# Kernel tuning notes

Measured on AMD Instinct MI355X. Metric: run time of the kernel, lower is better.

Reference implementation:

```python
import jax, jax.numpy as jnp
import numpy as np

WS = (4, 4, 4)      # window size (d, h, w)
SS = (2, 2, 2)      # shift size
HEADS = 4
EPS = 1e-6          # flax LayerNorm default epsilon


def _rel_pos_index(ws):
    # replicates the source exactly (np.meshgrid default 'xy' indexing)
    coords = np.stack(np.meshgrid(np.arange(ws[0]), np.arange(ws[1]), np.arange(ws[2])))
    cf = coords.reshape(3, -1)
    rc = (cf[:, :, None] - cf[:, None, :]).transpose(1, 2, 0).astype(np.int64)
    rc[:, :, 0] += ws[0] - 1
    rc[:, :, 1] += ws[1] - 1
    rc[:, :, 2] += ws[2] - 1
    rc[:, :, 0] *= (2 * ws[1] - 1) * (2 * ws[2] - 1)
    rc[:, :, 1] *= 2 * ws[2] - 1
    return rc.sum(-1)  # (n, n)


def _compute_mask(dp, hp, wp, ws, ss):
    # standard shifted-window attention mask: (nw, n, n) with 0 / -100
    img = np.zeros((1, dp, hp, wp, 1), np.float32)
    cnt = 0
    sls = lambda w, s: (slice(0, -w), slice(-w, -s), slice(-s, None))
    for d in sls(ws[0], ss[0]):
        for h in sls(ws[1], ss[1]):
            for w in sls(ws[2], ss[2]):
                img[:, d, h, w, :] = cnt
                cnt += 1
    mw = img.reshape(1, dp // ws[0], ws[0], hp // ws[1], ws[1], wp // ws[2], ws[2], 1)
    mw = mw.transpose(0, 1, 3, 5, 2, 4, 6, 7).reshape(-1, ws[0] * ws[1] * ws[2])
    am = mw[:, None, :] - mw[:, :, None]
    return np.where(am != 0, np.float32(-100.0), np.float32(0.0))


def window_partition(x, ws):
    b, d, h, w, c = x.shape
    x = x.reshape(b, d // ws[0], ws[0], h // ws[1], ws[1], w // ws[2], ws[2], c)
    return x.transpose(0, 1, 3, 5, 2, 4, 6, 7).reshape(-1, ws[0] * ws[1] * ws[2], c)


def window_reverse(windows, ws, dims):
    b, d, h, w = dims
    x = windows.reshape(b, d // ws[0], h // ws[1], w // ws[2], ws[0], ws[1], ws[2], -1)
    return x.transpose(0, 1, 4, 2, 5, 3, 6, 7).reshape(b, d, h, w, -1)


def layernorm(x, scale, bias):
    m = x.mean(-1, keepdims=True)
    v = x.var(-1, keepdims=True)
    return (x - m) * jax.lax.rsqrt(v + EPS) * scale + bias


def setup_inputs() -> dict:
    key = jax.random.key(0)
    ks = jax.random.split(key, 8)
    B, D, H, W, C = 2, 32, 64, 64, 128
    HID = 4 * C
    p = 0.02
    return {
        "x": jax.random.normal(ks[0], (B, D, H, W, C), jnp.float32),
        "mask": jnp.asarray(_compute_mask(D, H, W, WS, SS)),
        "norm1_scale": jnp.ones((C,), jnp.float32),
        "norm1_bias": jnp.zeros((C,), jnp.float32),
        "qkv_w": jax.random.normal(ks[1], (C, 3 * C), jnp.float32) * p,
        "rel_bias_table": jax.random.normal(ks[2], ((2 * WS[0] - 1) * (2 * WS[1] - 1) * (2 * WS[2] - 1), HEADS), jnp.float32) * p,
        "proj_w": jax.random.normal(ks[3], (C, C), jnp.float32) * p,
        "proj_b": jnp.zeros((C,), jnp.float32),
        "norm2_scale": jnp.ones((C,), jnp.float32),
        "norm2_bias": jnp.zeros((C,), jnp.float32),
        "mlp_w1": jax.random.normal(ks[4], (C, HID), jnp.float32) * p,
        "mlp_b1": jnp.zeros((HID,), jnp.float32),
        "mlp_w2": jax.random.normal(ks[5], (HID, C), jnp.float32) * p,
        "mlp_b2": jnp.zeros((C,), jnp.float32),
    }


def reference(x, mask, norm1_scale, norm1_bias, qkv_w, rel_bias_table, proj_w, proj_b,
              norm2_scale, norm2_bias, mlp_w1, mlp_b1, mlp_w2, mlp_b2):
    b, d, h, w, c = x.shape
    hd = c // HEADS
    scale = hd ** -0.5
    n = WS[0] * WS[1] * WS[2]

    shortcut = x
    xn = layernorm(x, norm1_scale, norm1_bias)
    # cyclic shift + window partition
    shifted = jnp.roll(xn, shift=(-SS[0], -SS[1], -SS[2]), axis=(1, 2, 3))
    xw = window_partition(shifted, WS)                      # (b*nw, n, c)
    bw = xw.shape[0]

    qkv = (xw @ qkv_w).reshape(bw, n, 3, HEADS, hd).transpose(2, 0, 3, 1, 4)
    q, k, v = qkv[0] * scale, qkv[1], qkv[2]                # (bw, heads, n, hd)
    attn = jnp.einsum('bhqd,bhkd->bhqk', q, k)              # (bw, heads, n, n)

    idx = _rel_pos_index(WS)
    bias = rel_bias_table[idx.reshape(-1)].reshape(n, n, HEADS).transpose(2, 0, 1)
    attn = attn + bias[None]

    nw = mask.shape[0]
    attn = attn.reshape(bw // nw, nw, HEADS, n, n) + mask[None, :, None]
    attn = jax.nn.softmax(attn.reshape(bw, HEADS, n, n), axis=-1)

    out = jnp.einsum('bhqk,bhkd->bhqd', attn, v)
    out = jnp.swapaxes(out, 1, 2).reshape(bw, n, c)
    out = out @ proj_w + proj_b

    attn_out = window_reverse(out, WS, (b, d, h, w))
    attn_out = jnp.roll(attn_out, shift=SS, axis=(1, 2, 3))

    x = shortcut + attn_out
    xn2 = layernorm(x, norm2_scale, norm2_bias)
    m = jax.nn.gelu(xn2 @ mlp_w1 + mlp_b1) @ mlp_w2 + mlp_b2
    return x + m
```

## Files before the change

kernel.cpp:

```cpp
#include <hip/hip_runtime.h>

typedef __bf16 bf16x8 __attribute__((ext_vector_type(8)));
typedef float f32x4 __attribute__((ext_vector_type(4)));
typedef unsigned short u16x4 __attribute__((ext_vector_type(4)));
typedef unsigned short u16x8 __attribute__((ext_vector_type(8)));

#define MFMA16(a,b,c) __builtin_amdgcn_mfma_f32_16x16x32_bf16((a),(b),(c),0,0,0)

__device__ __forceinline__ unsigned short f2bf(float f){
  return __builtin_bit_cast(unsigned short, static_cast<__bf16>(f));
}
__device__ __forceinline__ float bf2f(unsigned short h){
  unsigned u = ((unsigned)h)<<16;
  return __builtin_bit_cast(float, u);
}
__device__ __forceinline__ bf16x8 g_frag(const unsigned short* __restrict__ wf, int fragIdx, int lane){
  return __builtin_bit_cast(bf16x8, *reinterpret_cast<const u16x8*>(wf + (size_t)(fragIdx*64 + lane)*8));
}
__device__ __forceinline__ bf16x8 lds_frag(const unsigned short* base, int fragIdx, int lane){
  return __builtin_bit_cast(bf16x8, *reinterpret_cast<const u16x8*>(base + (fragIdx*64 + lane)*8));
}
__device__ __forceinline__ bf16x8 bc(u16x8 v){ return __builtin_bit_cast(bf16x8, v); }

__device__ __forceinline__ void pack_body(const float* __restrict__ src, unsigned short* __restrict__ dst,
                                          int blk, int MT, int KP, int M){
  int tid = blk*256 + threadIdx.x;
  if (tid >= MT*KP*64) return;
  int lane = tid & 63;
  int t2 = tid >> 6;
  int kp = t2 % KP;
  int m = 16*(t2 / KP) + (lane & 15);
  int g = lane >> 4;
  u16x8 v;
#pragma unroll
  for (int j = 0; j < 8; ++j) {
    int k = 4*g + (j&3) + 16*(j>>2) + 32*kp;
    v[j] = f2bf(src[k*M + m]);
  }
  *reinterpret_cast<u16x8*>(&dst[(size_t)tid*8]) = v;
}

__global__ void prep_kernel(const float* __restrict__ qkvw, const float* __restrict__ pw,
                            const float* __restrict__ w1, const float* __restrict__ w2,
                            const float* __restrict__ tbl,
                            unsigned short* __restrict__ wqk_f, unsigned short* __restrict__ wvb_f,
                            unsigned short* __restrict__ wproj_f,
                            unsigned short* __restrict__ w1_f, unsigned short* __restrict__ w2_f,
                            float* __restrict__ bias2){
  const int bb = blockIdx.x;
  if (bb < 16)      { pack_body(qkvw,       wqk_f,   bb,      16, 4, 384); return; }
  else if (bb < 24) { pack_body(qkvw + 256, wvb_f,   bb-16,    8, 4, 384); return; }
  else if (bb < 32) { pack_body(pw,         wproj_f, bb-24,    8, 4, 128); return; }
  else if (bb < 64) { pack_body(w1,         w1_f,    bb-32,   32, 4, 512); return; }
  else if (bb < 96) { pack_body(w2,         w2_f,    bb-64,    8,16, 128); return; }
  const int o = (bb-96)*256 + threadIdx.x;
  int r2 = o&3, lane = (o>>2)&63, nt = (o>>8)&3, mt = (o>>10)&3, h = o>>12;
  int g = lane>>4, l15 = lane&15;
  int key = 16*mt + 4*g + r2, q = 16*nt + l15;
  int da = ((q>>2)&3) - ((key>>2)&3) + 3;
  int ha = (q>>4)     - (key>>4)     + 3;
  int wa = (q&3)      - (key&3)      + 3;
  bias2[o] = tbl[((da*7+ha)*7+wa)*4 + h];
}

__global__ __launch_bounds__(256, 3)
void swin_block_kernel(const float* __restrict__ x,
                       const float* __restrict__ n1s, const float* __restrict__ n1b,
                       const unsigned short* __restrict__ wqk,
                       const unsigned short* __restrict__ wvb,
                       const float* __restrict__ bias2,
                       const unsigned short* __restrict__ wproj,
                       const float* __restrict__ projb,
                       const float* __restrict__ n2s, const float* __restrict__ n2b,
                       const unsigned short* __restrict__ w1f, const float* __restrict__ b1,
                       const unsigned short* __restrict__ w2f, const float* __restrict__ b2,
                       float* __restrict__ out)
{
  __shared__ __align__(16) unsigned short ldsA[16*64*8];
  __shared__ __align__(16) unsigned short ldsH[16*64*8];
  __shared__ int rid_s[64];

  const int tid  = threadIdx.x;
  const int lane = tid & 63;
  const int w    = tid >> 6;
  const int g    = lane >> 4;
  const int l15  = lane & 15;

  const int wb = blockIdx.x;
  const int b  = wb >> 11;
  const int r0 = wb & 2047;
  const int bd = r0 >> 8, bh = (r0 >> 4) & 15, bwi = r0 & 15;
  const bool edge = (bd==7) || (bh==15) || (bwi==15);

  const int t = tid >> 2, qtr = tid & 3;
  const int wd = t >> 4, wh = (t >> 2) & 3, ww = t & 3;
  const int dco = (bd*4 + wd + 2) & 31;
  const int hco = (bh*4 + wh + 2) & 63;
  const int wco = (bwi*4 + ww + 2) & 63;
  const long tokl = ((long)((b*32 + dco)*64 + hco))*64 + wco;
  const float* xrow = x + tokl*128 + qtr*32;
  const int tileT = t >> 4, l15t = t & 15;

  u16x8 rsd[4];
  {
    float xr[32];
    float s = 0.f, sq = 0.f;
#pragma unroll
    for (int i = 0; i < 8; ++i) {
      float4 v = reinterpret_cast<const float4*>(xrow)[i];
      xr[4*i+0]=v.x; xr[4*i+1]=v.y; xr[4*i+2]=v.z; xr[4*i+3]=v.w;
      s  += v.x + v.y + v.z + v.w;
      sq += v.x*v.x + v.y*v.y + v.z*v.z + v.w*v.w;
    }
    s  += __shfl_xor(s, 1);  s  += __shfl_xor(s, 2);
    sq += __shfl_xor(sq, 1); sq += __shfl_xor(sq, 2);
    const float mean = s * 0.0078125f;
    const float rs   = rsqrtf(sq * 0.0078125f - mean*mean + 1e-6f);
#pragma unroll
    for (int i = 0; i < 8; ++i) {
      u16x4 o4;
#pragma unroll
      for (int j2 = 0; j2 < 4; ++j2) {
        int c = qtr*32 + 4*i + j2;
        o4[j2] = f2bf((xr[4*i+j2]-mean)*rs*n1s[c] + n1b[c]);
        rsd[i>>1][4*(i&1)+j2] = f2bf(xr[4*i+j2]);
      }
      *reinterpret_cast<u16x4*>(&ldsA[((tileT*4+qtr)*64 + l15t + 16*(i&3))*8 + 4*(i>>2)]) = o4;
    }
  }
  if (edge && tid < 64) {
    int twd = tid >> 4, twh = (tid >> 2) & 3, tww = tid & 3;
    int rd = (bd == 7)  ? (twd < 2 ? 1 : 2) : 0;
    int rh = (bh == 15) ? (twh < 2 ? 1 : 2) : 0;
    int rw = (bwi == 15)? (tww < 2 ? 1 : 2) : 0;
    rid_s[tid] = rd*9 + rh*3 + rw;
  }
  __syncthreads();

  u16x8 Qf[4], Kf[4], Vf[2][2];
  {
    f32x4 qacc[2][4], kacc[2][4], vacc[4][2];
#pragma unroll
    for (int a2=0;a2<2;++a2)
#pragma unroll
      for (int b4=0;b4<4;++b4){ f32x4 z={0.f,0.f,0.f,0.f}; qacc[a2][b4]=z; kacc[a2][b4]=z; vacc[b4][a2]=z; }
#pragma unroll
    for (int kp=0;kp<4;++kp){
      bf16x8 fx[4];
#pragma unroll
      for (int nt=0;nt<4;++nt) fx[nt] = lds_frag(ldsA, nt*4+kp, lane);
#pragma unroll
      for (int mi=0;mi<2;++mi){
        bf16x8 aq = g_frag(wqk, (2*w+mi)*4+kp, lane);
#pragma unroll
        for (int nt=0;nt<4;++nt) qacc[mi][nt] = MFMA16(aq, fx[nt], qacc[mi][nt]);
      }
#pragma unroll
      for (int mi=0;mi<2;++mi){
        bf16x8 ak = g_frag(wqk, (8+2*w+mi)*4+kp, lane);
#pragma unroll
        for (int nt=0;nt<4;++nt) kacc[mi][nt] = MFMA16(ak, fx[nt], kacc[mi][nt]);
      }
#pragma unroll
      for (int c2=0;c2<2;++c2){
        bf16x8 bv = g_frag(wvb, (2*w+c2)*4+kp, lane);
#pragma unroll
        for (int mt=0;mt<4;++mt) vacc[mt][c2] = MFMA16(fx[mt], bv, vacc[mt][c2]);
      }
    }
#pragma unroll
    for (int nt=0;nt<4;++nt){
      u16x8 vq, vk;
#pragma unroll
      for (int j=0;j<8;++j){
        vq[j] = f2bf(qacc[j>>2][nt][j&3]*0.17677669529663687f);
        vk[j] = f2bf(kacc[j>>2][nt][j&3]);
      }
      Qf[nt]=vq; Kf[nt]=vk;
    }
#pragma unroll
    for (int c2=0;c2<2;++c2)
#pragma unroll
      for (int kpk=0;kpk<2;++kpk){
        u16x8 v;
#pragma unroll
        for (int j=0;j<8;++j) v[j] = f2bf(vacc[(j>>2)+2*kpk][c2][j&3]);
        Vf[c2][kpk]=v;
      }
  }
  __syncthreads();

  {
    int4 rk[4];
    if (edge){
#pragma unroll
      for (int mt=0;mt<4;++mt) rk[mt] = *reinterpret_cast<const int4*>(&rid_s[16*mt + 4*g]);
    }
#pragma unroll
    for (int nt=0;nt<4;++nt){
      f32x4 sacc[4];
#pragma unroll
      for (int mt=0;mt<4;++mt){
        f32x4 z = {0.f,0.f,0.f,0.f};
        sacc[mt] = MFMA16(bc(Kf[mt]), bc(Qf[nt]), z);
      }
      if (edge){
        const int ridq = rid_s[16*nt + l15];
#pragma unroll
        for (int mt=0;mt<4;++mt){
          float4 bv = reinterpret_cast<const float4*>(bias2)[((w*4+mt)*4+nt)*64 + lane];
          sacc[mt][0] += bv.x + (rk[mt].x != ridq ? -100.f : 0.f);
          sacc[mt][1] += bv.y + (rk[mt].y != ridq ? -100.f : 0.f);
          sacc[mt][2] += bv.z + (rk[mt].z != ridq ? -100.f : 0.f);
          sacc[mt][3] += bv.w + (rk[mt].w != ridq ? -100.f : 0.f);
        }
      } else {
#pragma unroll
        for (int mt=0;mt<4;++mt){
          float4 bv = reinterpret_cast<const float4*>(bias2)[((w*4+mt)*4+nt)*64 + lane];
          sacc[mt][0] += bv.x; sacc[mt][1] += bv.y; sacc[mt][2] += bv.z; sacc[mt][3] += bv.w;
        }
      }
      float mx = -1e30f;
#pragma unroll
      for (int mt=0;mt<4;++mt)
#pragma unroll
        for (int r2=0;r2<4;++r2) mx = fmaxf(mx, sacc[mt][r2]);
      mx = fmaxf(mx, __shfl_xor(mx, 16));
      mx = fmaxf(mx, __shfl_xor(mx, 32));
      float sum = 0.f;
#pragma unroll
      for (int mt=0;mt<4;++mt)
#pragma unroll
        for (int r2=0;r2<4;++r2){
          float p = __expf(sacc[mt][r2] - mx);
          sacc[mt][r2] = p; sum += p;
        }
      sum += __shfl_xor(sum, 16);
      sum += __shfl_xor(sum, 32);
      const float inv = 1.f / sum;
      u16x8 Pf0, Pf1;
#pragma unroll
      for (int j=0;j<8;++j){
        Pf0[j] = f2bf(sacc[(j>>2)  ][j&3]*inv);
        Pf1[j] = f2bf(sacc[(j>>2)+2][j&3]*inv);
      }
      f32x4 oa[2];
#pragma unroll
      for (int c2=0;c2<2;++c2){
        f32x4 z = {0.f,0.f,0.f,0.f};
        z = MFMA16(bc(Vf[c2][0]), bc(Pf0), z);
        oa[c2] = MFMA16(bc(Vf[c2][1]), bc(Pf1), z);
      }
      u16x8 v;
#pragma unroll
      for (int j=0;j<8;++j) v[j] = f2bf(oa[j>>2][j&3]);
      *reinterpret_cast<u16x8*>(&ldsA[((nt*4+w)*64+lane)*8]) = v;
    }
  }
  __syncthreads();

  {
    f32x4 pacc[2][4];
#pragma unroll
    for (int mi=0;mi<2;++mi)
#pragma unroll
      for (int nt=0;nt<4;++nt){ f32x4 z={0.f,0.f,0.f,0.f}; pacc[mi][nt]=z; }
#pragma unroll
    for (int kp=0;kp<4;++kp){
      bf16x8 bo[4];
#pragma unroll
      for (int nt=0;nt<4;++nt) bo[nt] = lds_frag(ldsA, nt*4+kp, lane);
#pragma unroll
      for (int mi=0;mi<2;++mi){
        bf16x8 a = g_frag(wproj, (2*w+mi)*4+kp, lane);
#pragma unroll
        for (int nt=0;nt<4;++nt) pacc[mi][nt] = MFMA16(a, bo[nt], pacc[mi][nt]);
      }
    }
#pragma unroll
    for (int mi=0;mi<2;++mi)
#pragma unroll
      for (int r2=0;r2<4;++r2){
        const float pb = projb[16*(2*w+mi) + 4*g + r2];
#pragma unroll
        for (int nt=0;nt<4;++nt) pacc[mi][nt][r2] += pb;
      }
#pragma unroll
    for (int nt=0;nt<4;++nt){
      u16x8 v;
#pragma unroll
      for (int j=0;j<8;++j) v[j] = f2bf(pacc[j>>2][nt][j&3]);
      *reinterpret_cast<u16x8*>(&ldsH[((nt*4+w)*64+lane)*8]) = v;
    }
  }
  __syncthreads();

  {
    float xv[32];
    float s2 = 0.f, sq2 = 0.f;
#pragma unroll
    for (int i = 0; i < 8; ++i) {
      u16x4 sg = *reinterpret_cast<const u16x4*>(&ldsH[((tileT*4+qtr)*64 + l15t + 16*(i&3))*8 + 4*(i>>2)]);
#pragma unroll
      for (int j2 = 0; j2 < 4; ++j2) {
        float v2 = bf2f(rsd[i>>1][4*(i&1)+j2]) + bf2f(sg[j2]);
        xv[4*i+j2] = v2;
        s2 += v2; sq2 += v2*v2;
      }
    }
    s2  += __shfl_xor(s2, 1);  s2  += __shfl_xor(s2, 2);
    sq2 += __shfl_xor(sq2, 1); sq2 += __shfl_xor(sq2, 2);
    const float mean2 = s2*0.0078125f;
    const float rs2 = rsqrtf(sq2*0.0078125f - mean2*mean2 + 1e-6f);
#pragma unroll
    for (int i = 0; i < 8; ++i) {
      u16x4 o4;
#pragma unroll
      for (int j2 = 0; j2 < 4; ++j2) {
        int c = qtr*32 + 4*i + j2;
        o4[j2] = f2bf((xv[4*i+j2]-mean2)*rs2*n2s[c] + n2b[c]);
        rsd[i>>1][4*(i&1)+j2] = f2bf(xv[4*i+j2]);
      }
      *reinterpret_cast<u16x4*>(&ldsA[((tileT*4+qtr)*64 + l15t + 16*(i&3))*8 + 4*(i>>2)]) = o4;
    }
  }
  __syncthreads();

  {
    f32x4 macc[2][4];
#pragma unroll
    for (int mi=0;mi<2;++mi)
#pragma unroll
      for (int nt=0;nt<4;++nt){ f32x4 z={0.f,0.f,0.f,0.f}; macc[mi][nt]=z; }
#pragma unroll
    for (int cc=0;cc<4;++cc){
      f32x4 hacc[2][4];
#pragma unroll
      for (int mi=0;mi<2;++mi)
#pragma unroll
        for (int nt=0;nt<4;++nt){ f32x4 z={0.f,0.f,0.f,0.f}; hacc[mi][nt]=z; }
#pragma unroll
      for (int kp=0;kp<4;++kp){
        bf16x8 bn[4];
#pragma unroll
        for (int nt=0;nt<4;++nt) bn[nt] = lds_frag(ldsA, nt*4+kp, lane);
#pragma unroll
        for (int mi=0;mi<2;++mi){
          bf16x8 a = g_frag(w1f, (cc*8+2*w+mi)*4+kp, lane);
#pragma unroll
          for (int nt=0;nt<4;++nt) hacc[mi][nt] = MFMA16(a, bn[nt], hacc[mi][nt]);
        }
      }
#pragma unroll
      for (int nt=0;nt<4;++nt){
        u16x8 hv;
#pragma unroll
        for (int j=0;j<8;++j){
          const int mi = j>>2, r2 = j&3;
          const int hch = cc*128 + 32*w + 16*mi + 4*g + r2;
          float v2 = hacc[mi][nt][r2] + b1[hch];
          float gg = 0.7978845608028654f*(v2 + 0.044715f*v2*v2*v2);
          float ge = v2 / (1.f + __expf(-2.f*gg));
          hv[j] = f2bf(ge);
        }
        *reinterpret_cast<u16x8*>(&ldsH[((nt*4+w)*64+lane)*8]) = hv;
      }
      __syncthreads();
#pragma unroll
      for (int kph=0;kph<4;++kph){
        bf16x8 bhf[4];
#pragma unroll
        for (int nt=0;nt<4;++nt) bhf[nt] = lds_frag(ldsH, nt*4+kph, lane);
#pragma unroll
        for (int mi=0;mi<2;++mi){
          bf16x8 a2 = g_frag(w2f, (2*w+mi)*16 + cc*4 + kph, lane);
#pragma unroll
          for (int nt=0;nt<4;++nt) macc[mi][nt] = MFMA16(a2, bhf[nt], macc[mi][nt]);
        }
      }
      __syncthreads();
    }
#pragma unroll
    for (int nt=0;nt<4;++nt){
      u16x8 v;
#pragma unroll
      for (int j=0;j<8;++j){
        const int mi = j>>2, r2 = j&3;
        v[j] = f2bf(macc[mi][nt][r2] + b2[16*(2*w+mi) + 4*g + r2]);
      }
      *reinterpret_cast<u16x8*>(&ldsA[((nt*4+w)*64+lane)*8]) = v;
    }
  }
  __syncthreads();

  {
    float* orow = out + tokl*128 + qtr*32;
#pragma unroll
    for (int i = 0; i < 8; ++i) {
      u16x4 mv = *reinterpret_cast<const u16x4*>(&ldsA[((tileT*4+qtr)*64 + l15t + 16*(i&3))*8 + 4*(i>>2)]);
      float4 v;
      v.x = bf2f(rsd[i>>1][4*(i&1)+0]) + bf2f(mv[0]);
      v.y = bf2f(rsd[i>>1][4*(i&1)+1]) + bf2f(mv[1]);
      v.z = bf2f(rsd[i>>1][4*(i&1)+2]) + bf2f(mv[2]);
      v.w = bf2f(rsd[i>>1][4*(i&1)+3]) + bf2f(mv[3]);
      reinterpret_cast<float4*>(orow)[i] = v;
    }
  }
}

extern "C" void kernel_launch(void* const* d_in, const int* in_sizes, int n_in,
                              void* d_out, int out_size, void* d_ws, size_t ws_size,
                              hipStream_t stream) {
  (void)in_sizes; (void)n_in; (void)out_size; (void)ws_size;
  const float* x    = (const float*)d_in[0];
  const float* n1s  = (const float*)d_in[2];
  const float* n1b  = (const float*)d_in[3];
  const float* qkvw = (const float*)d_in[4];
  const float* tbl  = (const float*)d_in[5];
  const float* pw   = (const float*)d_in[6];
  const float* pb   = (const float*)d_in[7];
  const float* n2s  = (const float*)d_in[8];
  const float* n2b  = (const float*)d_in[9];
  const float* w1   = (const float*)d_in[10];
  const float* b1   = (const float*)d_in[11];
  const float* w2   = (const float*)d_in[12];
  const float* b2   = (const float*)d_in[13];
  float* out = (float*)d_out;

  unsigned short* wqk_f   = (unsigned short*)d_ws;
  unsigned short* wvb_f   = wqk_f   + 16*4*64*8;
  unsigned short* wproj_f = wvb_f   + 8*4*64*8;
  unsigned short* w1_f    = wproj_f + 8*4*64*8;
  unsigned short* w2_f    = w1_f    + 32*4*64*8;
  float*          bias2   = (float*)(w2_f + 8*16*64*8);

  prep_kernel<<<160, 256, 0, stream>>>(qkvw, pw, w1, w2, tbl,
                                       wqk_f, wvb_f, wproj_f, w1_f, w2_f, bias2);

  swin_block_kernel<<<4096, 256, 0, stream>>>(x, n1s, n1b, wqk_f, wvb_f, bias2, wproj_f, pb,
                                              n2s, n2b, w1_f, b1, w2_f, b2, out);
}
```

Before: 552.1 us.

## Split QKV projection into sequential phases and fold q-scale into weights

The fused Q/K/V projection loop, which held 24 accumulator tiles live at once, becomes three sequential phases that reuse one accumulator set, separated by scheduling barriers. The aim is to cut peak register pressure. The attention scale is folded into the packed Q weights during prep, so the kernel no longer multiplies per element. Launch bounds drop from 3 to 2 waves per EU, giving the compiler more registers at the cost of occupancy, and the LDS fragments are now reloaded three times instead of once.

```diff
diff --git a/kernel.cpp b/kernel.cpp
--- a/kernel.cpp
+++ b/kernel.cpp
@@ -23,7 +23,7 @@
 __device__ __forceinline__ bf16x8 bc(u16x8 v){ return __builtin_bit_cast(bf16x8, v); }
 
 __device__ __forceinline__ void pack_body(const float* __restrict__ src, unsigned short* __restrict__ dst,
-                                          int blk, int MT, int KP, int M){
+                                          int blk, int MT, int KP, int M, float scale){
   int tid = blk*256 + threadIdx.x;
   if (tid >= MT*KP*64) return;
   int lane = tid & 63;
@@ -35,7 +35,7 @@
 #pragma unroll
   for (int j = 0; j < 8; ++j) {
     int k = 4*g + (j&3) + 16*(j>>2) + 32*kp;
-    v[j] = f2bf(src[k*M + m]);
+    v[j] = f2bf(scale*src[k*M + m]);
   }
   *reinterpret_cast<u16x8*>(&dst[(size_t)tid*8]) = v;
 }
@@ -48,11 +48,12 @@
                             unsigned short* __restrict__ w1_f, unsigned short* __restrict__ w2_f,
                             float* __restrict__ bias2){
   const int bb = blockIdx.x;
-  if (bb < 16)      { pack_body(qkvw,       wqk_f,   bb,      16, 4, 384); return; }
-  else if (bb < 24) { pack_body(qkvw + 256, wvb_f,   bb-16,    8, 4, 384); return; }
-  else if (bb < 32) { pack_body(pw,         wproj_f, bb-24,    8, 4, 128); return; }
-  else if (bb < 64) { pack_body(w1,         w1_f,    bb-32,   32, 4, 512); return; }
-  else if (bb < 96) { pack_body(w2,         w2_f,    bb-64,    8,16, 128); return; }
+  if (bb < 8)       { pack_body(qkvw,       wqk_f,   bb,      16, 4, 384, 0.17677669529663687f); return; }
+  else if (bb < 16) { pack_body(qkvw,       wqk_f,   bb,      16, 4, 384, 1.f); return; }
+  else if (bb < 24) { pack_body(qkvw + 256, wvb_f,   bb-16,    8, 4, 384, 1.f); return; }
+  else if (bb < 32) { pack_body(pw,         wproj_f, bb-24,    8, 4, 128, 1.f); return; }
+  else if (bb < 64) { pack_body(w1,         w1_f,    bb-32,   32, 4, 512, 1.f); return; }
+  else if (bb < 96) { pack_body(w2,         w2_f,    bb-64,    8,16, 128, 1.f); return; }
   const int o = (bb-96)*256 + threadIdx.x;
   int r2 = o&3, lane = (o>>2)&63, nt = (o>>8)&3, mt = (o>>10)&3, h = o>>12;
   int g = lane>>4, l15 = lane&15;
@@ -63,7 +64,7 @@
   bias2[o] = tbl[((da*7+ha)*7+wa)*4 + h];
 }
 
-__global__ __launch_bounds__(256, 3)
+__global__ __launch_bounds__(256, 2)
 void swin_block_kernel(const float* __restrict__ x,
                        const float* __restrict__ n1s, const float* __restrict__ n1b,
                        const unsigned short* __restrict__ wqk,
@@ -139,11 +140,11 @@
 
   u16x8 Qf[4], Kf[4], Vf[2][2];
   {
-    f32x4 qacc[2][4], kacc[2][4], vacc[4][2];
-#pragma unroll
-    for (int a2=0;a2<2;++a2)
-#pragma unroll
-      for (int b4=0;b4<4;++b4){ f32x4 z={0.f,0.f,0.f,0.f}; qacc[a2][b4]=z; kacc[a2][b4]=z; vacc[b4][a2]=z; }
+    f32x4 acc[2][4];
+#pragma unroll
+    for (int mi=0;mi<2;++mi)
+#pragma unroll
+      for (int nt=0;nt<4;++nt){ f32x4 z={0.f,0.f,0.f,0.f}; acc[mi][nt]=z; }
 #pragma unroll
     for (int kp=0;kp<4;++kp){
       bf16x8 fx[4];
@@ -151,16 +152,53 @@
       for (int nt=0;nt<4;++nt) fx[nt] = lds_frag(ldsA, nt*4+kp, lane);
 #pragma unroll
       for (int mi=0;mi<2;++mi){
-        bf16x8 aq = g_frag(wqk, (2*w+mi)*4+kp, lane);
-#pragma unroll
-        for (int nt=0;nt<4;++nt) qacc[mi][nt] = MFMA16(aq, fx[nt], qacc[mi][nt]);
-      }
+        bf16x8 a = g_frag(wqk, (2*w+mi)*4+kp, lane);
+#pragma unroll
+        for (int nt=0;nt<4;++nt) acc[mi][nt] = MFMA16(a, fx[nt], acc[mi][nt]);
+      }
+    }
+#pragma unroll
+    for (int nt=0;nt<4;++nt){
+      u16x8 v;
+#pragma unroll
+      for (int j=0;j<8;++j) v[j] = f2bf(acc[j>>2][nt][j&3]);
+      Qf[nt]=v;
+    }
+    __builtin_amdgcn_sched_barrier(0);
+#pragma unroll
+    for (int mi=0;mi<2;++mi)
+#pragma unroll
+      for (int nt=0;nt<4;++nt){ f32x4 z={0.f,0.f,0.f,0.f}; acc[mi][nt]=z; }
+#pragma unroll
+    for (int kp=0;kp<4;++kp){
+      bf16x8 fx[4];
+#pragma unroll
+      for (int nt=0;nt<4;++nt) fx[nt] = lds_frag(ldsA, nt*4+kp, lane);
 #pragma unroll
       for (int mi=0;mi<2;++mi){
-        bf16x8 ak = g_frag(wqk, (8+2*w+mi)*4+kp, lane);
-#pragma unroll
-        for (int nt=0;nt<4;++nt) kacc[mi][nt] = MFMA16(ak, fx[nt], kacc[mi][nt]);
-      }
+        bf16x8 a = g_frag(wqk, (8+2*w+mi)*4+kp, lane);
+#pragma unroll
+        for (int nt=0;nt<4;++nt) acc[mi][nt] = MFMA16(a, fx[nt], acc[mi][nt]);
+      }
+    }
+#pragma unroll
+    for (int nt=0;nt<4;++nt){
+      u16x8 v;
+#pragma unroll
+      for (int j=0;j<8;++j) v[j] = f2bf(acc[j>>2][nt][j&3]);
+      Kf[nt]=v;
+    }
+    __builtin_amdgcn_sched_barrier(0);
+    f32x4 vacc[4][2];
+#pragma unroll
+    for (int mt=0;mt<4;++mt)
+#pragma unroll
+      for (int c2=0;c2<2;++c2){ f32x4 z={0.f,0.f,0.f,0.f}; vacc[mt][c2]=z; }
+#pragma unroll
+    for (int kp=0;kp<4;++kp){
+      bf16x8 fx[4];
+#pragma unroll
+      for (int mt=0;mt<4;++mt) fx[mt] = lds_frag(ldsA, mt*4+kp, lane);
 #pragma unroll
       for (int c2=0;c2<2;++c2){
         bf16x8 bv = g_frag(wvb, (2*w+c2)*4+kp, lane);
@@ -169,16 +207,6 @@
       }
     }
 #pragma unroll
-    for (int nt=0;nt<4;++nt){
-      u16x8 vq, vk;
-#pragma unroll
-      for (int j=0;j<8;++j){
-        vq[j] = f2bf(qacc[j>>2][nt][j&3]*0.17677669529663687f);
-        vk[j] = f2bf(kacc[j>>2][nt][j&3]);
-      }
-      Qf[nt]=vq; Kf[nt]=vk;
-    }
-#pragma unroll
     for (int c2=0;c2<2;++c2)
 #pragma unroll
       for (int kpk=0;kpk<2;++kpk){
@@ -187,6 +215,7 @@
         for (int j=0;j<8;++j) v[j] = f2bf(vacc[(j>>2)+2*kpk][c2][j&3]);
         Vf[c2][kpk]=v;
       }
+    __builtin_amdgcn_sched_barrier(0);
   }
   __syncthreads();
 
```

Measured after the change: 481.1 us. -12.9%, faster.
